# Optimization experiments

Measured on AMD Instinct MI355X. Metric: run time of the kernel, lower is better.

## Reference

```python
import jax, jax.numpy as jnp
import numpy as np

B, C, F = 8, 2048, 128


def setup_inputs() -> dict:
    key = jax.random.key(0)
    ks = jax.random.split(key, 13)
    features = jax.random.normal(ks[0], (B, C, F), dtype=jnp.float32)
    # sparse-ish boolean adjacency masks over operations
    pred_mask = jax.random.uniform(ks[1], (B, C, C)) < 0.05
    succ_mask = jax.random.uniform(ks[2], (B, C, C)) < 0.05
    same_type_mask = jax.random.uniform(ks[3], (B, C, C)) < 0.10

    def linear(k, fan_in, fan_out):
        kw, kb = jax.random.split(k)
        bound = 1.0 / np.sqrt(fan_in)
        W = jax.random.uniform(kw, (fan_in, fan_out), minval=-bound, maxval=bound, dtype=jnp.float32)
        b = jax.random.uniform(kb, (fan_out,), minval=-bound, maxval=bound, dtype=jnp.float32)
        return W, b

    W_enc, b_enc = linear(ks[4], F, 4 * F)
    W_space, b_space = linear(ks[5], 3 * F, F)
    W_same, b_same = linear(ks[6], 2 * F, F)
    W_mix, b_mix = linear(ks[7], 2 * F, F)
    return {
        "features": features,
        "pred_mask": pred_mask,
        "succ_mask": succ_mask,
        "same_type_mask": same_type_mask,
        "W_enc": W_enc, "b_enc": b_enc,
        "W_space": W_space, "b_space": b_space,
        "W_same": W_same, "b_same": b_same,
        "W_mix": W_mix, "b_mix": b_mix,
    }


def reference(features, pred_mask, succ_mask, same_type_mask,
              W_enc, b_enc, W_space, b_space, W_same, b_same, W_mix, b_mix):
    # encoder: [B,C,F] -> [B,C,4F], split into origin + 3 message features
    enc = features @ W_enc + b_enc
    origin, e_pred, e_succ, e_same = jnp.split(enc, 4, axis=-1)

    def masked_mean(mask, e):
        # original builds (B,C,C,F) broadcast product then sums over 'other';
        # mathematically this is mask @ e with a clamped-degree divisor.
        m = mask.astype(e.dtype)                         # [B,C,C]
        deg = jnp.maximum(m.sum(-1, keepdims=True), 1.0)  # [B,C,1]
        return jnp.einsum('bij,bjf->bif', m, e) / deg

    pred_f = masked_mean(pred_mask, e_pred)
    succ_f = masked_mean(succ_mask, e_succ)
    same_f = masked_mean(same_type_mask, e_same)

    space_mixed = jnp.concatenate([pred_f, origin, succ_f], axis=-1) @ W_space + b_space
    same_mixed = jnp.concatenate([origin, same_f], axis=-1) @ W_same + b_same
    return jnp.concatenate([space_mixed, same_mixed], axis=-1) @ W_mix + b_mix
```

## Files before the change

### kernel.cpp

```cpp
#include <hip/hip_runtime.h>
#include <stdint.h>

typedef unsigned int uint;
typedef unsigned short ushort;
typedef unsigned char uchar;
typedef __attribute__((ext_vector_type(8))) short bf16x8;
typedef __attribute__((ext_vector_type(4))) float f32x4;

__device__ __forceinline__ ushort f2bf(float f) {
  uint u = __builtin_bit_cast(uint, f);
  return (ushort)((u + 0x7FFFu + ((u >> 16) & 1u)) >> 16);
}

__device__ __forceinline__ bf16x8 cvt8(uint lo, uint hi, uint& cacc) {
  uint x0 = __builtin_amdgcn_perm(0u, lo, 0x04010400u);
  uint x1 = __builtin_amdgcn_perm(0u, lo, 0x04030402u);
  uint x2 = __builtin_amdgcn_perm(0u, hi, 0x04010400u);
  uint x3 = __builtin_amdgcn_perm(0u, hi, 0x04030402u);
  uint n0 = ((x0 + 0x00FF00FFu) >> 8) & 0x00010001u;
  uint n1 = ((x1 + 0x00FF00FFu) >> 8) & 0x00010001u;
  uint n2 = ((x2 + 0x00FF00FFu) >> 8) & 0x00010001u;
  uint n3 = ((x3 + 0x00FF00FFu) >> 8) & 0x00010001u;
  cacc += n0 + n1 + n2 + n3;
  uint4 o;
  o.x = n0 * 0x3F80u; o.y = n1 * 0x3F80u;
  o.z = n2 * 0x3F80u; o.w = n3 * 0x3F80u;
  return __builtin_bit_cast(bf16x8, o);
}

__device__ __forceinline__ bf16x8 cvt8w(uint4 a, uint4 b, uint& cnt) {
  bf16x8 r;
  r[0] = a.x ? (short)0x3F80 : (short)0; cnt += (a.x != 0u);
  r[1] = a.y ? (short)0x3F80 : (short)0; cnt += (a.y != 0u);
  r[2] = a.z ? (short)0x3F80 : (short)0; cnt += (a.z != 0u);
  r[3] = a.w ? (short)0x3F80 : (short)0; cnt += (a.w != 0u);
  r[4] = b.x ? (short)0x3F80 : (short)0; cnt += (b.x != 0u);
  r[5] = b.y ? (short)0x3F80 : (short)0; cnt += (b.y != 0u);
  r[6] = b.z ? (short)0x3F80 : (short)0; cnt += (b.z != 0u);
  r[7] = b.w ? (short)0x3F80 : (short)0; cnt += (b.w != 0u);
  return r;
}

__global__ __launch_bounds__(256) void k_detect(
    const uint4* __restrict__ m, int* __restrict__ esz_out) {
  __shared__ int s_ok;
  if (threadIdx.x == 0) s_ok = 1;
  __syncthreads();
  int ok = 1;
#pragma unroll
  for (int i = 0; i < 16; ++i) {
    uint4 v = m[i * 256 + threadIdx.x];
    if (!(v.x <= 1u || v.x == 0x3F800000u)) ok = 0;
    if (!(v.y <= 1u || v.y == 0x3F800000u)) ok = 0;
    if (!(v.z <= 1u || v.z == 0x3F800000u)) ok = 0;
    if (!(v.w <= 1u || v.w == 0x3F800000u)) ok = 0;
  }
  if (!ok) atomicAnd(&s_ok, 0);
  __syncthreads();
  if (threadIdx.x == 0) *esz_out = s_ok ? 4 : 1;
}

__global__ __launch_bounds__(256) void k_prep(
    const float4* __restrict__ fin, ushort* __restrict__ fout,
    const float* __restrict__ We, const float* __restrict__ Ws,
    const float* __restrict__ Wm, const float* __restrict__ Wx,
    ushort* __restrict__ Te, ushort* __restrict__ Ts,
    ushort* __restrict__ Tm, ushort* __restrict__ Tx) {
  const int tid = blockIdx.x * 256 + threadIdx.x;
  for (int i = tid; i < 524288; i += 180224) {
    float4 v = fin[i];
    ushort4 o;
    o.x = f2bf(v.x); o.y = f2bf(v.y); o.z = f2bf(v.z); o.w = f2bf(v.w);
    *(ushort4*)&fout[(size_t)i * 4] = o;
  }
  int i = tid;
  if (i < 65536) { int n = i >> 7, k = i & 127; Te[i] = f2bf(We[k * 512 + n]); return; }
  i -= 65536;
  if (i < 49152) { int n = i / 384, k = i - n * 384; Ts[i] = f2bf(Ws[k * 128 + n]); return; }
  i -= 49152;
  if (i < 32768) { int n = i >> 8, k = i & 255; Tm[i] = f2bf(Wm[k * 128 + n]); return; }
  i -= 32768;
  if (i < 32768) { int n = i >> 8, k = i & 255; Tx[i] = f2bf(Wx[k * 128 + n]); return; }
}

__global__ __launch_bounds__(256) void k_enc(
    const ushort* __restrict__ featbf, const ushort* __restrict__ WTe,
    const float* __restrict__ bias, ushort* __restrict__ origin,
    ushort* __restrict__ eT0, ushort* __restrict__ eT1, ushort* __restrict__ eT2) {
  const int t = threadIdx.x;
  const int gm0 = blockIdx.x * 64;
  const int y = blockIdx.y;
  const int lane = t & 63, wave = t >> 6;
  const int m0w = (wave >> 1) * 32, n0w = (wave & 1) * 64;
  const int quad = lane >> 4, lr = lane & 15;
  const ushort* a0p = featbf + (size_t)(gm0 + m0w + lr) * 128 + quad * 8;
  const ushort* a1p = a0p + 16 * 128;
  bf16x8 af0[4], af1[4];
#pragma unroll
  for (int kc = 0; kc < 4; ++kc) {
    af0[kc] = *(const bf16x8*)(a0p + kc * 32);
    af1[kc] = *(const bf16x8*)(a1p + kc * 32);
  }
  f32x4 acc[2][4] = {};
#pragma unroll
  for (int j = 0; j < 4; ++j) {
    const ushort* bp = WTe + (size_t)(y * 128 + n0w + j * 16 + lr) * 128 + quad * 8;
#pragma unroll
    for (int kc = 0; kc < 4; ++kc) {
      bf16x8 bv = *(const bf16x8*)(bp + kc * 32);
      acc[0][j] = __builtin_amdgcn_mfma_f32_16x16x32_bf16(af0[kc], bv, acc[0][j], 0, 0, 0);
      acc[1][j] = __builtin_amdgcn_mfma_f32_16x16x32_bf16(af1[kc], bv, acc[1][j], 0, 0, 0);
    }
  }
  if (y == 0) {
#pragma unroll
    for (int i = 0; i < 2; ++i)
#pragma unroll
      for (int j = 0; j < 4; ++j) {
        int n = n0w + j * 16 + lr;
        float bb = bias[n];
        int mb = gm0 + m0w + i * 16 + quad * 4;
#pragma unroll
        for (int r = 0; r < 4; ++r)
          origin[(size_t)(mb + r) * 128 + n] = f2bf(acc[i][j][r] + bb);
      }
  } else {
    ushort* eT = (y == 1) ? eT0 : (y == 2) ? eT1 : eT2;
#pragma unroll
    for (int i = 0; i < 2; ++i)
#pragma unroll
      for (int j = 0; j < 4; ++j) {
        int n = n0w + j * 16 + lr;
        float bb = bias[y * 128 + n];
        int mb = gm0 + m0w + i * 16 + quad * 4;
        ushort4 o;
        o.x = f2bf(acc[i][j][0] + bb);
        o.y = f2bf(acc[i][j][1] + bb);
        o.z = f2bf(acc[i][j][2] + bb);
        o.w = f2bf(acc[i][j][3] + bb);
        *(ushort4*)&eT[(size_t)n * 16384 + mb] = o;
      }
  }
}

__global__ __launch_bounds__(256, 3) void k_mm(
    const void* __restrict__ mp, const void* __restrict__ ms,
    const void* __restrict__ mt,
    const ushort* __restrict__ eT0, const ushort* __restrict__ eT1,
    const ushort* __restrict__ eT2,
    ushort* __restrict__ P, ushort* __restrict__ S, ushort* __restrict__ T,
    const int* __restrict__ esz_p) {
  __shared__ uint degs[64];
  const int t = threadIdx.x;
  const int mtile = blockIdx.x, b = blockIdx.y, mid = blockIdx.z;
  const void* mask = (mid == 0) ? mp : (mid == 1) ? ms : mt;
  const ushort* eT = (mid == 0) ? eT0 : (mid == 1) ? eT1 : eT2;
  ushort* outp = (mid == 0) ? P : (mid == 1) ? S : T;
  const int esz = *esz_p;
  const size_t rowbase = (size_t)b * 2048 + mtile * 64;
  const int lane = t & 63, wave = t >> 6;
  const int m0w = (wave >> 1) * 32, n0w = (wave & 1) * 64;
  const int quad = lane >> 4, lr = lane & 15;
  const int r0 = m0w + lr, r1 = m0w + 16 + lr;
  const ushort* bp0 = eT + (size_t)(n0w + lr) * 16384 + (size_t)b * 2048 + quad * 8;
  const ushort* bp1 = bp0 + 16 * 16384;
  const ushort* bp2 = bp0 + 32 * 16384;
  const ushort* bp3 = bp0 + 48 * 16384;
  f32x4 acc[2][4] = {};
  uint cacc0 = 0, cacc1 = 0;

  if (esz == 1) {
    const uchar* ma = (const uchar*)mask + (rowbase + r0) * 2048 + quad * 8;
    const uchar* mb = (const uchar*)mask + (rowbase + r1) * 2048 + quad * 8;
    uint2 ra0 = *(const uint2*)(ma);
    uint2 ra1 = *(const uint2*)(ma + 32);
    uint2 rb0 = *(const uint2*)(mb);
    uint2 rb1 = *(const uint2*)(mb + 32);
#pragma unroll 2
    for (int k0 = 0; k0 < 2048; k0 += 64) {
      uint2 na0 = {}, na1 = {}, nb0 = {}, nb1 = {};
      if (k0 + 64 < 2048) {
        na0 = *(const uint2*)(ma + k0 + 64);
        na1 = *(const uint2*)(ma + k0 + 96);
        nb0 = *(const uint2*)(mb + k0 + 64);
        nb1 = *(const uint2*)(mb + k0 + 96);
      }
#pragma unroll
      for (int kc = 0; kc < 2; ++kc) {
        bf16x8 bv0 = *(const bf16x8*)(bp0 + k0 + kc * 32);
        bf16x8 bv1 = *(const bf16x8*)(bp1 + k0 + kc * 32);
        bf16x8 bv2 = *(const bf16x8*)(bp2 + k0 + kc * 32);
        bf16x8 bv3 = *(const bf16x8*)(bp3 + k0 + kc * 32);
        uint2 wa = kc ? ra1 : ra0;
        uint2 wb = kc ? rb1 : rb0;
        bf16x8 a0 = cvt8(wa.x, wa.y, cacc0);
        bf16x8 a1 = cvt8(wb.x, wb.y, cacc1);
        acc[0][0] = __builtin_amdgcn_mfma_f32_16x16x32_bf16(a0, bv0, acc[0][0], 0, 0, 0);
        acc[1][0] = __builtin_amdgcn_mfma_f32_16x16x32_bf16(a1, bv0, acc[1][0], 0, 0, 0);
        acc[0][1] = __builtin_amdgcn_mfma_f32_16x16x32_bf16(a0, bv1, acc[0][1], 0, 0, 0);
        acc[1][1] = __builtin_amdgcn_mfma_f32_16x16x32_bf16(a1, bv1, acc[1][1], 0, 0, 0);
        acc[0][2] = __builtin_amdgcn_mfma_f32_16x16x32_bf16(a0, bv2, acc[0][2], 0, 0, 0);
        acc[1][2] = __builtin_amdgcn_mfma_f32_16x16x32_bf16(a1, bv2, acc[1][2], 0, 0, 0);
        acc[0][3] = __builtin_amdgcn_mfma_f32_16x16x32_bf16(a0, bv3, acc[0][3], 0, 0, 0);
        acc[1][3] = __builtin_amdgcn_mfma_f32_16x16x32_bf16(a1, bv3, acc[1][3], 0, 0, 0);
      }
      ra0 = na0; ra1 = na1; rb0 = nb0; rb1 = nb1;
    }
  } else {
    const uint* ma = (const uint*)mask + (rowbase + r0) * 2048 + quad * 8;
    const uint* mb = (const uint*)mask + (rowbase + r1) * 2048 + quad * 8;
    for (int k0 = 0; k0 < 2048; k0 += 64) {
#pragma unroll
      for (int kc = 0; kc < 2; ++kc) {
        uint4 wa0 = *(const uint4*)(ma + k0 + kc * 32);
        uint4 wa1 = *(const uint4*)(ma + k0 + kc * 32 + 4);
        uint4 wb0 = *(const uint4*)(mb + k0 + kc * 32);
        uint4 wb1 = *(const uint4*)(mb + k0 + kc * 32 + 4);
        bf16x8 bv0 = *(const bf16x8*)(bp0 + k0 + kc * 32);
        bf16x8 bv1 = *(const bf16x8*)(bp1 + k0 + kc * 32);
        bf16x8 bv2 = *(const bf16x8*)(bp2 + k0 + kc * 32);
        bf16x8 bv3 = *(const bf16x8*)(bp3 + k0 + kc * 32);
        bf16x8 a0 = cvt8w(wa0, wa1, cacc0);
        bf16x8 a1 = cvt8w(wb0, wb1, cacc1);
        acc[0][0] = __builtin_amdgcn_mfma_f32_16x16x32_bf16(a0, bv0, acc[0][0], 0, 0, 0);
        acc[1][0] = __builtin_amdgcn_mfma_f32_16x16x32_bf16(a1, bv0, acc[1][0], 0, 0, 0);
        acc[0][1] = __builtin_amdgcn_mfma_f32_16x16x32_bf16(a0, bv1, acc[0][1], 0, 0, 0);
        acc[1][1] = __builtin_amdgcn_mfma_f32_16x16x32_bf16(a1, bv1, acc[1][1], 0, 0, 0);
        acc[0][2] = __builtin_amdgcn_mfma_f32_16x16x32_bf16(a0, bv2, acc[0][2], 0, 0, 0);
        acc[1][2] = __builtin_amdgcn_mfma_f32_16x16x32_bf16(a1, bv2, acc[1][2], 0, 0, 0);
        acc[0][3] = __builtin_amdgcn_mfma_f32_16x16x32_bf16(a0, bv3, acc[0][3], 0, 0, 0);
        acc[1][3] = __builtin_amdgcn_mfma_f32_16x16x32_bf16(a1, bv3, acc[1][3], 0, 0, 0);
      }
    }
  }

  int c0, c1;
  if (esz == 1) {
    c0 = (int)((cacc0 & 0xFFFFu) + (cacc0 >> 16));
    c1 = (int)((cacc1 & 0xFFFFu) + (cacc1 >> 16));
  } else {
    c0 = (int)cacc0;
    c1 = (int)cacc1;
  }
  c0 += __shfl_xor(c0, 16); c0 += __shfl_xor(c0, 32);
  c1 += __shfl_xor(c1, 16); c1 += __shfl_xor(c1, 32);
  if ((wave & 1) == 0 && quad == 0) { degs[r0] = (uint)c0; degs[r1] = (uint)c1; }
  __syncthreads();

#pragma unroll
  for (int i = 0; i < 2; ++i)
#pragma unroll
    for (int r = 0; r < 4; ++r) {
      int ml = m0w + i * 16 + quad * 4 + r;
      uint d = degs[ml];
      float inv = 1.0f / (float)(d > 0u ? d : 1u);
#pragma unroll
      for (int j = 0; j < 4; ++j) {
        int n = n0w + j * 16 + lr;
        outp[(rowbase + ml) * 128 + n] = f2bf(acc[i][j][r] * inv);
      }
    }
}

__device__ __forceinline__ void gemm_body(
    const ushort* __restrict__ A0, const ushort* __restrict__ A1,
    const ushort* __restrict__ A2, const ushort* __restrict__ Bsrc,
    int bstride, int K, const float* __restrict__ bias,
    void* __restrict__ out, int out_f32, int gm0, int t) {
  const int lane = t & 63, wave = t >> 6;
  const int m0w = (wave >> 1) * 32, n0w = (wave & 1) * 64;
  const int quad = lane >> 4, lr = lane & 15;
  const ushort* bbase = Bsrc + (size_t)(n0w + lr) * bstride + quad * 8;
  f32x4 acc[2][4] = {};
  for (int k0 = 0; k0 < K; k0 += 64) {
    const int seg = k0 >> 7;
    const ushort* Ap = (seg == 0) ? A0 : (seg == 1) ? A1 : A2;
    const int ko = k0 & 127;
    const ushort* a0p = Ap + (size_t)(gm0 + m0w + lr) * 128 + ko + quad * 8;
    const ushort* a1p = a0p + 16 * 128;
#pragma unroll
    for (int kc = 0; kc < 2; ++kc) {
      bf16x8 av0 = *(const bf16x8*)(a0p + kc * 32);
      bf16x8 av1 = *(const bf16x8*)(a1p + kc * 32);
      bf16x8 b0 = *(const bf16x8*)(bbase + k0 + kc * 32);
      bf16x8 b1 = *(const bf16x8*)(bbase + (size_t)16 * bstride + k0 + kc * 32);
      bf16x8 b2 = *(const bf16x8*)(bbase + (size_t)32 * bstride + k0 + kc * 32);
      bf16x8 b3 = *(const bf16x8*)(bbase + (size_t)48 * bstride + k0 + kc * 32);
      acc[0][0] = __builtin_amdgcn_mfma_f32_16x16x32_bf16(av0, b0, acc[0][0], 0, 0, 0);
      acc[1][0] = __builtin_amdgcn_mfma_f32_16x16x32_bf16(av1, b0, acc[1][0], 0, 0, 0);
      acc[0][1] = __builtin_amdgcn_mfma_f32_16x16x32_bf16(av0, b1, acc[0][1], 0, 0, 0);
      acc[1][1] = __builtin_amdgcn_mfma_f32_16x16x32_bf16(av1, b1, acc[1][1], 0, 0, 0);
      acc[0][2] = __builtin_amdgcn_mfma_f32_16x16x32_bf16(av0, b2, acc[0][2], 0, 0, 0);
      acc[1][2] = __builtin_amdgcn_mfma_f32_16x16x32_bf16(av1, b2, acc[1][2], 0, 0, 0);
      acc[0][3] = __builtin_amdgcn_mfma_f32_16x16x32_bf16(av0, b3, acc[0][3], 0, 0, 0);
      acc[1][3] = __builtin_amdgcn_mfma_f32_16x16x32_bf16(av1, b3, acc[1][3], 0, 0, 0);
    }
  }
#pragma unroll
  for (int i = 0; i < 2; ++i)
#pragma unroll
    for (int j = 0; j < 4; ++j) {
      const int n = n0w + j * 16 + lr;
      const float bb = bias[n];
      const int mb = gm0 + m0w + i * 16 + quad * 4;
      if (out_f32) {
#pragma unroll
        for (int r = 0; r < 4; ++r)
          ((float*)out)[(size_t)(mb + r) * 128 + n] = acc[i][j][r] + bb;
      } else {
#pragma unroll
        for (int r = 0; r < 4; ++r)
          ((ushort*)out)[(size_t)(mb + r) * 128 + n] = f2bf(acc[i][j][r] + bb);
      }
    }
}

__global__ __launch_bounds__(256) void k_xy(
    const ushort* __restrict__ P, const ushort* __restrict__ origin,
    const ushort* __restrict__ S, const ushort* __restrict__ T,
    const ushort* __restrict__ WTs, const ushort* __restrict__ WTm,
    const float* __restrict__ bs, const float* __restrict__ bm,
    ushort* __restrict__ X, ushort* __restrict__ Y) {
  const int gm0 = blockIdx.x * 64;
  if (blockIdx.y == 0)
    gemm_body(P, origin, S, WTs, 384, 384, bs, X, 0, gm0, threadIdx.x);
  else
    gemm_body(origin, T, nullptr, WTm, 256, 256, bm, Y, 0, gm0, threadIdx.x);
}

__global__ __launch_bounds__(256) void k_mix(
    const ushort* __restrict__ X, const ushort* __restrict__ Y,
    const ushort* __restrict__ WTx, const float* __restrict__ bx,
    float* __restrict__ out) {
  gemm_body(X, Y, nullptr, WTx, 256, 256, bx, out, 1, blockIdx.x * 64, threadIdx.x);
}

extern "C" void kernel_launch(void* const* d_in, const int* in_sizes, int n_in,
                              void* d_out, int out_size, void* d_ws,
                              size_t ws_size, hipStream_t stream) {
  const float* features = (const float*)d_in[0];
  const void* pred = d_in[1];
  const void* succ = d_in[2];
  const void* same = d_in[3];
  const float* W_enc = (const float*)d_in[4];
  const float* b_enc = (const float*)d_in[5];
  const float* W_space = (const float*)d_in[6];
  const float* b_space = (const float*)d_in[7];
  const float* W_same = (const float*)d_in[8];
  const float* b_same = (const float*)d_in[9];
  const float* W_mix = (const float*)d_in[10];
  const float* b_mix = (const float*)d_in[11];

  const size_t M = 16384;
  ushort* w = (ushort*)d_ws;
  ushort* feat_bf = w;  w += M * 128;
  ushort* WT_enc = w;   w += 512 * 128;
  ushort* WT_space = w; w += 128 * 384;
  ushort* WT_same = w;  w += 128 * 256;
  ushort* WT_mix = w;   w += 128 * 256;
  ushort* origin = w;   w += M * 128;
  ushort* eT0 = w;      w += M * 128;
  ushort* eT1 = w;      w += M * 128;
  ushort* eT2 = w;      w += M * 128;
  ushort* P = w;        w += M * 128;
  ushort* S = w;        w += M * 128;
  ushort* T = w;        w += M * 128;
  ushort* X = w;        w += M * 128;
  ushort* Y = w;        w += M * 128;
  int* esz = (int*)w;

  k_detect<<<1, 256, 0, stream>>>((const uint4*)pred, esz);
  k_prep<<<704, 256, 0, stream>>>((const float4*)features, feat_bf,
                                  W_enc, W_space, W_same, W_mix,
                                  WT_enc, WT_space, WT_same, WT_mix);
  k_enc<<<dim3(256, 4), 256, 0, stream>>>(feat_bf, WT_enc, b_enc,
                                          origin, eT0, eT1, eT2);
  k_mm<<<dim3(32, 8, 3), 256, 0, stream>>>(pred, succ, same, eT0, eT1, eT2,
                                           P, S, T, esz);
  k_xy<<<dim3(256, 2), 256, 0, stream>>>(P, origin, S, T, WT_space, WT_same,
                                         b_space, b_same, X, Y);
  k_mix<<<256, 256, 0, stream>>>(X, Y, WT_mix, b_mix, (float*)d_out);
}
```

Before: 500.3 us.

## Stage mask and embedding tiles through LDS with double-buffered async loads

The byte-mask path of k_mm now copies the B (transposed embedding) and A (mask) tiles into swizzled, double-buffered LDS using global_load_lds, and overlaps these loads with MFMA compute behind explicit waitcnt and barriers. The grid is flattened and remapped so that blocks sharing a panel are scheduled together, which should help L2 reuse. k_enc also transposes its output through swizzled LDS so the eT writes to global memory are coalesced. The cost is extra LDS use (about 36KB per block in k_mm), which may reduce occupancy, plus more barriers per iteration.

```diff
diff --git a/kernel.cpp b/kernel.cpp
--- a/kernel.cpp
+++ b/kernel.cpp
@@ -87,6 +87,7 @@
     const ushort* __restrict__ featbf, const ushort* __restrict__ WTe,
     const float* __restrict__ bias, ushort* __restrict__ origin,
     ushort* __restrict__ eT0, ushort* __restrict__ eT1, ushort* __restrict__ eT2) {
+  __shared__ ushort tr[128 * 64];
   const int t = threadIdx.x;
   const int gm0 = blockIdx.x * 64;
   const int y = blockIdx.y;
@@ -132,14 +133,25 @@
       for (int j = 0; j < 4; ++j) {
         int n = n0w + j * 16 + lr;
         float bb = bias[y * 128 + n];
-        int mb = gm0 + m0w + i * 16 + quad * 4;
+        int m_lo = m0w + i * 16 + quad * 4;
+        int chunk = m_lo >> 3;
+        int byteo = n * 128 + ((chunk ^ (n & 7)) << 4) + (m_lo & 7) * 2;
         ushort4 o;
         o.x = f2bf(acc[i][j][0] + bb);
         o.y = f2bf(acc[i][j][1] + bb);
         o.z = f2bf(acc[i][j][2] + bb);
         o.w = f2bf(acc[i][j][3] + bb);
-        *(ushort4*)&eT[(size_t)n * 16384 + mb] = o;
+        *(ushort4*)((char*)tr + byteo) = o;
       }
+    __syncthreads();
+    const int n = t >> 1, half = t & 1;
+    ushort* gp = eT + (size_t)n * 16384 + gm0 + half * 32;
+#pragma unroll
+    for (int cc = 0; cc < 4; ++cc) {
+      int c = half * 4 + cc;
+      uint4 v = *(const uint4*)((char*)tr + n * 128 + ((c ^ (n & 7)) << 4));
+      *(uint4*)&gp[cc * 8] = v;
+    }
   }
 }
 
@@ -150,9 +162,15 @@
     const ushort* __restrict__ eT2,
     ushort* __restrict__ P, ushort* __restrict__ S, ushort* __restrict__ T,
     const int* __restrict__ esz_p) {
+  __shared__ ushort Bs[2][8192];
+  __shared__ uchar As1[2][4096];
   __shared__ uint degs[64];
   const int t = threadIdx.x;
-  const int mtile = blockIdx.x, b = blockIdx.y, mid = blockIdx.z;
+  const int g = blockIdx.x;
+  const int X = g & 7, seq = g >> 3;
+  const int pl = seq >> 5, mtile = seq & 31;
+  const int panel = pl * 8 + X;
+  const int b = panel / 3, mid = panel - b * 3;
   const void* mask = (mid == 0) ? mp : (mid == 1) ? ms : mt;
   const ushort* eT = (mid == 0) ? eT0 : (mid == 1) ? eT1 : eT2;
   ushort* outp = (mid == 0) ? P : (mid == 1) ? S : T;
@@ -162,51 +180,112 @@
   const int m0w = (wave >> 1) * 32, n0w = (wave & 1) * 64;
   const int quad = lane >> 4, lr = lane & 15;
   const int r0 = m0w + lr, r1 = m0w + 16 + lr;
-  const ushort* bp0 = eT + (size_t)(n0w + lr) * 16384 + (size_t)b * 2048 + quad * 8;
-  const ushort* bp1 = bp0 + 16 * 16384;
-  const ushort* bp2 = bp0 + 32 * 16384;
-  const ushort* bp3 = bp0 + 48 * 16384;
   f32x4 acc[2][4] = {};
   uint cacc0 = 0, cacc1 = 0;
 
   if (esz == 1) {
-    const uchar* ma = (const uchar*)mask + (rowbase + r0) * 2048 + quad * 8;
-    const uchar* mb = (const uchar*)mask + (rowbase + r1) * 2048 + quad * 8;
-    uint2 ra0 = *(const uint2*)(ma);
-    uint2 ra1 = *(const uint2*)(ma + 32);
-    uint2 rb0 = *(const uint2*)(mb);
-    uint2 rb1 = *(const uint2*)(mb + 32);
-#pragma unroll 2
-    for (int k0 = 0; k0 < 2048; k0 += 64) {
-      uint2 na0 = {}, na1 = {}, nb0 = {}, nb1 = {};
-      if (k0 + 64 < 2048) {
-        na0 = *(const uint2*)(ma + k0 + 64);
-        na1 = *(const uint2*)(ma + k0 + 96);
-        nb0 = *(const uint2*)(mb + k0 + 64);
-        nb1 = *(const uint2*)(mb + k0 + 96);
-      }
-#pragma unroll
-      for (int kc = 0; kc < 2; ++kc) {
-        bf16x8 bv0 = *(const bf16x8*)(bp0 + k0 + kc * 32);
-        bf16x8 bv1 = *(const bf16x8*)(bp1 + k0 + kc * 32);
-        bf16x8 bv2 = *(const bf16x8*)(bp2 + k0 + kc * 32);
-        bf16x8 bv3 = *(const bf16x8*)(bp3 + k0 + kc * 32);
-        uint2 wa = kc ? ra1 : ra0;
-        uint2 wb = kc ? rb1 : rb0;
-        bf16x8 a0 = cvt8(wa.x, wa.y, cacc0);
-        bf16x8 a1 = cvt8(wb.x, wb.y, cacc1);
-        acc[0][0] = __builtin_amdgcn_mfma_f32_16x16x32_bf16(a0, bv0, acc[0][0], 0, 0, 0);
-        acc[1][0] = __builtin_amdgcn_mfma_f32_16x16x32_bf16(a1, bv0, acc[1][0], 0, 0, 0);
-        acc[0][1] = __builtin_amdgcn_mfma_f32_16x16x32_bf16(a0, bv1, acc[0][1], 0, 0, 0);
-        acc[1][1] = __builtin_amdgcn_mfma_f32_16x16x32_bf16(a1, bv1, acc[1][1], 0, 0, 0);
-        acc[0][2] = __builtin_amdgcn_mfma_f32_16x16x32_bf16(a0, bv2, acc[0][2], 0, 0, 0);
-        acc[1][2] = __builtin_amdgcn_mfma_f32_16x16x32_bf16(a1, bv2, acc[1][2], 0, 0, 0);
-        acc[0][3] = __builtin_amdgcn_mfma_f32_16x16x32_bf16(a0, bv3, acc[0][3], 0, 0, 0);
-        acc[1][3] = __builtin_amdgcn_mfma_f32_16x16x32_bf16(a1, bv3, acc[1][3], 0, 0, 0);
-      }
-      ra0 = na0; ra1 = na1; rb0 = nb0; rb1 = nb1;
-    }
+    const int cB = (lane & 7) ^ (lane >> 3);
+    const ushort* gsrcB = eT + (size_t)(wave * 32 + (lane >> 3)) * 16384 +
+                          (size_t)b * 2048 + cB * 8;
+    const int srow = wave * 16 + (lane >> 2);
+    const int cA = ((lane & 3) ^ (srow & 3)) << 4;
+    const uchar* gsrcA = (const uchar*)mask + (rowbase + srow) * 2048 + cA;
+    char* ldsB = (char*)Bs;
+    char* ldsA = (char*)As1;
+
+#define STAGEALL(BUF, K0)                                                     \
+  {                                                                           \
+    _Pragma("unroll") for (int ii = 0; ii < 4; ++ii)                          \
+        __builtin_amdgcn_global_load_lds(                                     \
+            (const __attribute__((address_space(1))) uint*)(gsrcB +           \
+                (size_t)ii * 131072 + (K0)),                                  \
+            (__attribute__((address_space(3))) uint*)(ldsB + (BUF) * 16384 +  \
+                wave * 4096 + ii * 1024 + lane * 16),                         \
+            16, 0, 0);                                                        \
+    __builtin_amdgcn_global_load_lds(                                         \
+        (const __attribute__((address_space(1))) uint*)(gsrcA + (K0)),        \
+        (__attribute__((address_space(3))) uint*)(ldsA + (BUF) * 4096 +       \
+            wave * 1024 + lane * 16),                                         \
+        16, 0, 0);                                                            \
+  }
+
+    const int s0 = quad ^ (lr & 7);
+    const int rowb0 = (n0w + 0 * 16 + lr) * 128 + (s0 << 4);
+    const int rowb1 = (n0w + 1 * 16 + lr) * 128 + (s0 << 4);
+    const int rowb2 = (n0w + 2 * 16 + lr) * 128 + (s0 << 4);
+    const int rowb3 = (n0w + 3 * 16 + lr) * 128 + (s0 << 4);
+    const int aA0 = r0 * 64 + ((((quad >> 1) ^ (lr & 3))) << 4) + (quad & 1) * 8;
+    const int aB0 = aA0 + 16 * 64;
+
+#define COMPUTE(BUF)                                                          \
+  {                                                                           \
+    const char* bb = (const char*)Bs + (BUF) * 16384;                         \
+    const char* ab = (const char*)As1 + (BUF) * 4096;                         \
+    uint2 wa0 = *(const uint2*)(ab + aA0);                                    \
+    uint2 wa1 = *(const uint2*)(ab + (aA0 ^ 32));                             \
+    uint2 wb0 = *(const uint2*)(ab + aB0);                                    \
+    uint2 wb1 = *(const uint2*)(ab + (aB0 ^ 32));                             \
+    bf16x8 b00 = *(const bf16x8*)(bb + rowb0);                                \
+    bf16x8 b10 = *(const bf16x8*)(bb + rowb1);                                \
+    bf16x8 b20 = *(const bf16x8*)(bb + rowb2);                                \
+    bf16x8 b30 = *(const bf16x8*)(bb + rowb3);                                \
+    bf16x8 b01 = *(const bf16x8*)(bb + (rowb0 ^ 64));                         \
+    bf16x8 b11 = *(const bf16x8*)(bb + (rowb1 ^ 64));                         \
+    bf16x8 b21 = *(const bf16x8*)(bb + (rowb2 ^ 64));                         \
+    bf16x8 b31 = *(const bf16x8*)(bb + (rowb3 ^ 64));                         \
+    bf16x8 a0 = cvt8(wa0.x, wa0.y, cacc0);                                    \
+    bf16x8 a1 = cvt8(wb0.x, wb0.y, cacc1);                                    \
+    bf16x8 a0h = cvt8(wa1.x, wa1.y, cacc0);                                   \
+    bf16x8 a1h = cvt8(wb1.x, wb1.y, cacc1);                                   \
+    __builtin_amdgcn_s_setprio(1);                                            \
+    acc[0][0] = __builtin_amdgcn_mfma_f32_16x16x32_bf16(a0, b00, acc[0][0], 0, 0, 0); \
+    acc[1][0] = __builtin_amdgcn_mfma_f32_16x16x32_bf16(a1, b00, acc[1][0], 0, 0, 0); \
+    acc[0][1] = __builtin_amdgcn_mfma_f32_16x16x32_bf16(a0, b10, acc[0][1], 0, 0, 0); \
+    acc[1][1] = __builtin_amdgcn_mfma_f32_16x16x32_bf16(a1, b10, acc[1][1], 0, 0, 0); \
+    acc[0][2] = __builtin_amdgcn_mfma_f32_16x16x32_bf16(a0, b20, acc[0][2], 0, 0, 0); \
+    acc[1][2] = __builtin_amdgcn_mfma_f32_16x16x32_bf16(a1, b20, acc[1][2], 0, 0, 0); \
+    acc[0][3] = __builtin_amdgcn_mfma_f32_16x16x32_bf16(a0, b30, acc[0][3], 0, 0, 0); \
+    acc[1][3] = __builtin_amdgcn_mfma_f32_16x16x32_bf16(a1, b30, acc[1][3], 0, 0, 0); \
+    acc[0][0] = __builtin_amdgcn_mfma_f32_16x16x32_bf16(a0h, b01, acc[0][0], 0, 0, 0); \
+    acc[1][0] = __builtin_amdgcn_mfma_f32_16x16x32_bf16(a1h, b01, acc[1][0], 0, 0, 0); \
+    acc[0][1] = __builtin_amdgcn_mfma_f32_16x16x32_bf16(a0h, b11, acc[0][1], 0, 0, 0); \
+    acc[1][1] = __builtin_amdgcn_mfma_f32_16x16x32_bf16(a1h, b11, acc[1][1], 0, 0, 0); \
+    acc[0][2] = __builtin_amdgcn_mfma_f32_16x16x32_bf16(a0h, b21, acc[0][2], 0, 0, 0); \
+    acc[1][2] = __builtin_amdgcn_mfma_f32_16x16x32_bf16(a1h, b21, acc[1][2], 0, 0, 0); \
+    acc[0][3] = __builtin_amdgcn_mfma_f32_16x16x32_bf16(a0h, b31, acc[0][3], 0, 0, 0); \
+    acc[1][3] = __builtin_amdgcn_mfma_f32_16x16x32_bf16(a1h, b31, acc[1][3], 0, 0, 0); \
+    __builtin_amdgcn_s_setprio(0);                                            \
+  }
+
+#define KITER(BUF, VM)                                                        \
+  asm volatile("s_waitcnt vmcnt(" #VM ")" ::: "memory");                      \
+  __builtin_amdgcn_s_barrier();                                               \
+  __builtin_amdgcn_sched_barrier(0);                                          \
+  COMPUTE(BUF);                                                               \
+  asm volatile("" ::: "memory");                                              \
+  __builtin_amdgcn_s_barrier();
+
+    STAGEALL(0, 0)
+    STAGEALL(1, 64)
+    for (int k0 = 0; k0 < 1920; k0 += 128) {
+      KITER(0, 5)
+      STAGEALL(0, k0 + 128)
+      KITER(1, 5)
+      STAGEALL(1, k0 + 192)
+    }
+    KITER(0, 5)
+    asm volatile("s_waitcnt vmcnt(0)" ::: "memory");
+    __builtin_amdgcn_s_barrier();
+    __builtin_amdgcn_sched_barrier(0);
+    COMPUTE(1)
+#undef KITER
+#undef COMPUTE
+#undef STAGEALL
   } else {
+    const ushort* bp0 = eT + (size_t)(n0w + lr) * 16384 + (size_t)b * 2048 + quad * 8;
+    const ushort* bp1 = bp0 + 16 * 16384;
+    const ushort* bp2 = bp0 + 32 * 16384;
+    const ushort* bp3 = bp0 + 48 * 16384;
     const uint* ma = (const uint*)mask + (rowbase + r0) * 2048 + quad * 8;
     const uint* mb = (const uint*)mask + (rowbase + r1) * 2048 + quad * 8;
     for (int k0 = 0; k0 < 2048; k0 += 64) {
@@ -375,8 +454,8 @@
                                   WT_enc, WT_space, WT_same, WT_mix);
   k_enc<<<dim3(256, 4), 256, 0, stream>>>(feat_bf, WT_enc, b_enc,
                                           origin, eT0, eT1, eT2);
-  k_mm<<<dim3(32, 8, 3), 256, 0, stream>>>(pred, succ, same, eT0, eT1, eT2,
-                                           P, S, T, esz);
+  k_mm<<<768, 256, 0, stream>>>(pred, succ, same, eT0, eT1, eT2,
+                                P, S, T, esz);
   k_xy<<<dim3(256, 2), 256, 0, stream>>>(P, origin, S, T, WT_space, WT_same,
                                          b_space, b_same, X, Y);
   k_mix<<<256, 256, 0, stream>>>(X, Y, WT_mix, b_mix, (float*)d_out);
```

New measurement: 493.9 us. About the same (-1.3%).

## Split masked-mean GEMM into LDS-pipelined and register-pipelined kernels, stage encoder transpose

Applied to the files above, without the earlier changes.

The encoder now transposes its message outputs through a swizzled shared-memory tile, so each thread writes coalesced 16-byte chunks to the transposed eT buffers. The masked aggregation is split across two kernels, each handling half of the 24 batch-mask panels. The first uses global_load_lds into a triple-buffered, swizzled LDS pipeline with explicit waitcnt/barrier scheduling and raised MFMA priority. The second uses a double-buffered register prefetch of mask and embedding fragments. The aim is to hide global-load latency in the bandwidth-bound mask GEMM, at the cost of an extra kernel launch, two launches that run back to back rather than concurrently, and more LDS or register pressure.

```diff
diff --git a/kernel.cpp b/kernel.cpp
--- a/kernel.cpp
+++ b/kernel.cpp
@@ -87,6 +87,7 @@
     const ushort* __restrict__ featbf, const ushort* __restrict__ WTe,
     const float* __restrict__ bias, ushort* __restrict__ origin,
     ushort* __restrict__ eT0, ushort* __restrict__ eT1, ushort* __restrict__ eT2) {
+  __shared__ ushort tr[128 * 64];
   const int t = threadIdx.x;
   const int gm0 = blockIdx.x * 64;
   const int y = blockIdx.y;
@@ -132,18 +133,205 @@
       for (int j = 0; j < 4; ++j) {
         int n = n0w + j * 16 + lr;
         float bb = bias[y * 128 + n];
-        int mb = gm0 + m0w + i * 16 + quad * 4;
+        int m_lo = m0w + i * 16 + quad * 4;
+        int chunk = m_lo >> 3;
+        int byteo = n * 128 + ((chunk ^ (n & 7)) << 4) + (m_lo & 7) * 2;
         ushort4 o;
         o.x = f2bf(acc[i][j][0] + bb);
         o.y = f2bf(acc[i][j][1] + bb);
         o.z = f2bf(acc[i][j][2] + bb);
         o.w = f2bf(acc[i][j][3] + bb);
-        *(ushort4*)&eT[(size_t)n * 16384 + mb] = o;
+        *(ushort4*)((char*)tr + byteo) = o;
       }
-  }
-}
-
-__global__ __launch_bounds__(256, 3) void k_mm(
+    __syncthreads();
+    const int n = t >> 1, half = t & 1;
+    ushort* gp = eT + (size_t)n * 16384 + gm0 + half * 32;
+#pragma unroll
+    for (int cc = 0; cc < 4; ++cc) {
+      int c = half * 4 + cc;
+      uint4 v = *(const uint4*)((char*)tr + n * 128 + ((c ^ (n & 7)) << 4));
+      *(uint4*)&gp[cc * 8] = v;
+    }
+  }
+}
+
+__device__ __forceinline__ void mm_epilogue(
+    uint* degs, f32x4 acc[2][4], uint cacc0, uint cacc1, int esz,
+    int m0w, int n0w, int quad, int lr, int wave,
+    ushort* outp, size_t rowbase) {
+  const int r0 = m0w + lr, r1 = m0w + 16 + lr;
+  int c0, c1;
+  if (esz == 1) {
+    c0 = (int)((cacc0 & 0xFFFFu) + (cacc0 >> 16));
+    c1 = (int)((cacc1 & 0xFFFFu) + (cacc1 >> 16));
+  } else {
+    c0 = (int)cacc0;
+    c1 = (int)cacc1;
+  }
+  c0 += __shfl_xor(c0, 16); c0 += __shfl_xor(c0, 32);
+  c1 += __shfl_xor(c1, 16); c1 += __shfl_xor(c1, 32);
+  if ((wave & 1) == 0 && quad == 0) { degs[r0] = (uint)c0; degs[r1] = (uint)c1; }
+  __syncthreads();
+#pragma unroll
+  for (int i = 0; i < 2; ++i)
+#pragma unroll
+    for (int r = 0; r < 4; ++r) {
+      int ml = m0w + i * 16 + quad * 4 + r;
+      uint d = degs[ml];
+      float inv = 1.0f / (float)(d > 0u ? d : 1u);
+#pragma unroll
+      for (int j = 0; j < 4; ++j) {
+        int n = n0w + j * 16 + lr;
+        outp[(rowbase + ml) * 128 + n] = f2bf(acc[i][j][r] * inv);
+      }
+    }
+}
+
+__device__ __forceinline__ void mm_esz4(
+    const void* mask, const ushort* eT, size_t rowbase, int b,
+    int m0w, int n0w, int quad, int lr,
+    f32x4 acc[2][4], uint& cacc0, uint& cacc1) {
+  const int r0 = m0w + lr, r1 = m0w + 16 + lr;
+  const ushort* bp0 = eT + (size_t)(n0w + lr) * 16384 + (size_t)b * 2048 + quad * 8;
+  const ushort* bp1 = bp0 + 16 * 16384;
+  const ushort* bp2 = bp0 + 32 * 16384;
+  const ushort* bp3 = bp0 + 48 * 16384;
+  const uint* ma = (const uint*)mask + (rowbase + r0) * 2048 + quad * 8;
+  const uint* mb = (const uint*)mask + (rowbase + r1) * 2048 + quad * 8;
+  for (int k0 = 0; k0 < 2048; k0 += 64) {
+#pragma unroll
+    for (int kc = 0; kc < 2; ++kc) {
+      uint4 wa0 = *(const uint4*)(ma + k0 + kc * 32);
+      uint4 wa1 = *(const uint4*)(ma + k0 + kc * 32 + 4);
+      uint4 wb0 = *(const uint4*)(mb + k0 + kc * 32);
+      uint4 wb1 = *(const uint4*)(mb + k0 + kc * 32 + 4);
+      bf16x8 bv0 = *(const bf16x8*)(bp0 + k0 + kc * 32);
+      bf16x8 bv1 = *(const bf16x8*)(bp1 + k0 + kc * 32);
+      bf16x8 bv2 = *(const bf16x8*)(bp2 + k0 + kc * 32);
+      bf16x8 bv3 = *(const bf16x8*)(bp3 + k0 + kc * 32);
+      bf16x8 a0 = cvt8w(wa0, wa1, cacc0);
+      bf16x8 a1 = cvt8w(wb0, wb1, cacc1);
+      acc[0][0] = __builtin_amdgcn_mfma_f32_16x16x32_bf16(a0, bv0, acc[0][0], 0, 0, 0);
+      acc[1][0] = __builtin_amdgcn_mfma_f32_16x16x32_bf16(a1, bv0, acc[1][0], 0, 0, 0);
+      acc[0][1] = __builtin_amdgcn_mfma_f32_16x16x32_bf16(a0, bv1, acc[0][1], 0, 0, 0);
+      acc[1][1] = __builtin_amdgcn_mfma_f32_16x16x32_bf16(a1, bv1, acc[1][1], 0, 0, 0);
+      acc[0][2] = __builtin_amdgcn_mfma_f32_16x16x32_bf16(a0, bv2, acc[0][2], 0, 0, 0);
+      acc[1][2] = __builtin_amdgcn_mfma_f32_16x16x32_bf16(a1, bv2, acc[1][2], 0, 0, 0);
+      acc[0][3] = __builtin_amdgcn_mfma_f32_16x16x32_bf16(a0, bv3, acc[0][3], 0, 0, 0);
+      acc[1][3] = __builtin_amdgcn_mfma_f32_16x16x32_bf16(a1, bv3, acc[1][3], 0, 0, 0);
+    }
+  }
+}
+
+__global__ __launch_bounds__(256, 2) void k_mmA(
+    const void* __restrict__ mp, const void* __restrict__ ms,
+    const void* __restrict__ mt,
+    const ushort* __restrict__ eT0, const ushort* __restrict__ eT1,
+    const ushort* __restrict__ eT2,
+    ushort* __restrict__ P, ushort* __restrict__ S, ushort* __restrict__ T,
+    const int* __restrict__ esz_p) {
+  __shared__ __align__(16) char smem[61440];
+  const int t = threadIdx.x;
+  const int mtile = blockIdx.x;
+  const int panel = blockIdx.y;
+  const int b = panel / 3, mid = panel - b * 3;
+  const void* mask = (mid == 0) ? mp : (mid == 1) ? ms : mt;
+  const ushort* eT = (mid == 0) ? eT0 : (mid == 1) ? eT1 : eT2;
+  ushort* outp = (mid == 0) ? P : (mid == 1) ? S : T;
+  const int esz = *esz_p;
+  const size_t rowbase = (size_t)b * 2048 + mtile * 64;
+  const int lane = t & 63, wave = t >> 6;
+  const int m0w = (wave >> 1) * 32, n0w = (wave & 1) * 64;
+  const int quad = lane >> 4, lr = lane & 15;
+  f32x4 acc[2][4] = {};
+  uint cacc0 = 0, cacc1 = 0;
+
+  if (esz == 1) {
+    const int r0B = wave * 32 + (lane >> 3);
+    const ushort* gB = eT + (size_t)r0B * 16384 + (size_t)b * 2048 +
+                       ((lane & 7) ^ (r0B & 7)) * 8;
+    const int r0A = wave * 16 + (lane >> 2);
+    const uchar* gA = (const uchar*)mask + (size_t)(rowbase + r0A) * 2048 +
+                      (((lane & 3) ^ (r0A & 3)) << 4);
+
+#define STG(BUF, PH)                                                          \
+  {                                                                           \
+    _Pragma("unroll") for (int ii = 0; ii < 4; ++ii)                          \
+        __builtin_amdgcn_global_load_lds(                                     \
+            (const __attribute__((address_space(1))) uint*)(gB +              \
+                (size_t)ii * 8 * 16384 + (PH) * 64),                          \
+            (__attribute__((address_space(3))) uint*)(smem + (BUF) * 16384 +  \
+                wave * 4096 + ii * 1024 + lane * 16),                         \
+            16, 0, 0);                                                        \
+    __builtin_amdgcn_global_load_lds(                                         \
+        (const __attribute__((address_space(1))) uint*)(gA + (PH) * 64),      \
+        (__attribute__((address_space(3))) uint*)(smem + 49152 +              \
+            (BUF) * 4096 + wave * 1024 + lane * 16),                          \
+        16, 0, 0);                                                            \
+  }
+
+#define CPT(BUF)                                                              \
+  {                                                                           \
+    const char* Bb = smem + (BUF) * 16384;                                    \
+    const char* Ab = smem + 49152 + (BUF) * 4096;                             \
+    _Pragma("unroll") for (int kc = 0; kc < 2; ++kc) {                        \
+      const int ach = (((kc << 1) + (quad >> 1)) ^ (lr & 3)) << 4;            \
+      uint2 va0 = *(const uint2*)(Ab + (m0w + lr) * 64 + ach + (quad & 1) * 8); \
+      uint2 va1 = *(const uint2*)(Ab + (m0w + 16 + lr) * 64 + ach + (quad & 1) * 8); \
+      const int bch = (((kc << 2) + quad) ^ (lr & 7)) << 4;                   \
+      bf16x8 b0 = *(const bf16x8*)(Bb + (n0w + lr) * 128 + bch);              \
+      bf16x8 b1 = *(const bf16x8*)(Bb + (n0w + 16 + lr) * 128 + bch);         \
+      bf16x8 b2 = *(const bf16x8*)(Bb + (n0w + 32 + lr) * 128 + bch);         \
+      bf16x8 b3 = *(const bf16x8*)(Bb + (n0w + 48 + lr) * 128 + bch);         \
+      bf16x8 a0 = cvt8(va0.x, va0.y, cacc0);                                  \
+      bf16x8 a1 = cvt8(va1.x, va1.y, cacc1);                                  \
+      __builtin_amdgcn_s_setprio(1);                                          \
+      acc[0][0] = __builtin_amdgcn_mfma_f32_16x16x32_bf16(a0, b0, acc[0][0], 0, 0, 0); \
+      acc[1][0] = __builtin_amdgcn_mfma_f32_16x16x32_bf16(a1, b0, acc[1][0], 0, 0, 0); \
+      acc[0][1] = __builtin_amdgcn_mfma_f32_16x16x32_bf16(a0, b1, acc[0][1], 0, 0, 0); \
+      acc[1][1] = __builtin_amdgcn_mfma_f32_16x16x32_bf16(a1, b1, acc[1][1], 0, 0, 0); \
+      acc[0][2] = __builtin_amdgcn_mfma_f32_16x16x32_bf16(a0, b2, acc[0][2], 0, 0, 0); \
+      acc[1][2] = __builtin_amdgcn_mfma_f32_16x16x32_bf16(a1, b2, acc[1][2], 0, 0, 0); \
+      acc[0][3] = __builtin_amdgcn_mfma_f32_16x16x32_bf16(a0, b3, acc[0][3], 0, 0, 0); \
+      acc[1][3] = __builtin_amdgcn_mfma_f32_16x16x32_bf16(a1, b3, acc[1][3], 0, 0, 0); \
+      __builtin_amdgcn_s_setprio(0);                                          \
+    }                                                                         \
+  }
+
+#define ITER(BUF, VM)                                                         \
+  asm volatile("s_waitcnt vmcnt(" #VM ")" ::: "memory");                      \
+  __builtin_amdgcn_s_barrier();                                               \
+  __builtin_amdgcn_sched_barrier(0);                                          \
+  CPT(BUF);                                                                   \
+  asm volatile("" ::: "memory");                                              \
+  __builtin_amdgcn_s_barrier();                                               \
+  asm volatile("" ::: "memory");
+
+    STG(0, 0)
+    STG(1, 1)
+    STG(2, 2)
+    for (int ph = 0; ph < 27; ph += 3) {
+      ITER(0, 10) STG(0, ph + 3)
+      ITER(1, 10) STG(1, ph + 4)
+      ITER(2, 10) STG(2, ph + 5)
+    }
+    ITER(0, 10) STG(0, 30)
+    ITER(1, 10) STG(1, 31)
+    ITER(2, 10)
+    ITER(0, 5)
+    ITER(1, 0)
+#undef ITER
+#undef CPT
+#undef STG
+  } else {
+    mm_esz4(mask, eT, rowbase, b, m0w, n0w, quad, lr, acc, cacc0, cacc1);
+  }
+  __syncthreads();
+  mm_epilogue((uint*)smem, acc, cacc0, cacc1, esz, m0w, n0w, quad, lr, wave,
+              outp, rowbase);
+}
+
+__global__ __launch_bounds__(256, 3) void k_mmB(
     const void* __restrict__ mp, const void* __restrict__ ms,
     const void* __restrict__ mt,
     const ushort* __restrict__ eT0, const ushort* __restrict__ eT1,
@@ -152,7 +340,9 @@
     const int* __restrict__ esz_p) {
   __shared__ uint degs[64];
   const int t = threadIdx.x;
-  const int mtile = blockIdx.x, b = blockIdx.y, mid = blockIdx.z;
+  const int mtile = blockIdx.x;
+  const int panel = 12 + blockIdx.y;
+  const int b = panel / 3, mid = panel - b * 3;
   const void* mask = (mid == 0) ? mp : (mid == 1) ? ms : mt;
   const ushort* eT = (mid == 0) ? eT0 : (mid == 1) ? eT1 : eT2;
   ushort* outp = (mid == 0) ? P : (mid == 1) ? S : T;
@@ -161,105 +351,79 @@
   const int lane = t & 63, wave = t >> 6;
   const int m0w = (wave >> 1) * 32, n0w = (wave & 1) * 64;
   const int quad = lane >> 4, lr = lane & 15;
-  const int r0 = m0w + lr, r1 = m0w + 16 + lr;
-  const ushort* bp0 = eT + (size_t)(n0w + lr) * 16384 + (size_t)b * 2048 + quad * 8;
-  const ushort* bp1 = bp0 + 16 * 16384;
-  const ushort* bp2 = bp0 + 32 * 16384;
-  const ushort* bp3 = bp0 + 48 * 16384;
   f32x4 acc[2][4] = {};
   uint cacc0 = 0, cacc1 = 0;
 
   if (esz == 1) {
+    const int r0 = m0w + lr, r1 = m0w + 16 + lr;
     const uchar* ma = (const uchar*)mask + (rowbase + r0) * 2048 + quad * 8;
     const uchar* mb = (const uchar*)mask + (rowbase + r1) * 2048 + quad * 8;
-    uint2 ra0 = *(const uint2*)(ma);
-    uint2 ra1 = *(const uint2*)(ma + 32);
-    uint2 rb0 = *(const uint2*)(mb);
-    uint2 rb1 = *(const uint2*)(mb + 32);
-#pragma unroll 2
-    for (int k0 = 0; k0 < 2048; k0 += 64) {
-      uint2 na0 = {}, na1 = {}, nb0 = {}, nb1 = {};
-      if (k0 + 64 < 2048) {
-        na0 = *(const uint2*)(ma + k0 + 64);
-        na1 = *(const uint2*)(ma + k0 + 96);
-        nb0 = *(const uint2*)(mb + k0 + 64);
-        nb1 = *(const uint2*)(mb + k0 + 96);
-      }
-#pragma unroll
-      for (int kc = 0; kc < 2; ++kc) {
-        bf16x8 bv0 = *(const bf16x8*)(bp0 + k0 + kc * 32);
-        bf16x8 bv1 = *(const bf16x8*)(bp1 + k0 + kc * 32);
-        bf16x8 bv2 = *(const bf16x8*)(bp2 + k0 + kc * 32);
-        bf16x8 bv3 = *(const bf16x8*)(bp3 + k0 + kc * 32);
-        uint2 wa = kc ? ra1 : ra0;
-        uint2 wb = kc ? rb1 : rb0;
-        bf16x8 a0 = cvt8(wa.x, wa.y, cacc0);
-        bf16x8 a1 = cvt8(wb.x, wb.y, cacc1);
-        acc[0][0] = __builtin_amdgcn_mfma_f32_16x16x32_bf16(a0, bv0, acc[0][0], 0, 0, 0);
-        acc[1][0] = __builtin_amdgcn_mfma_f32_16x16x32_bf16(a1, bv0, acc[1][0], 0, 0, 0);
-        acc[0][1] = __builtin_amdgcn_mfma_f32_16x16x32_bf16(a0, bv1, acc[0][1], 0, 0, 0);
-        acc[1][1] = __builtin_amdgcn_mfma_f32_16x16x32_bf16(a1, bv1, acc[1][1], 0, 0, 0);
-        acc[0][2] = __builtin_amdgcn_mfma_f32_16x16x32_bf16(a0, bv2, acc[0][2], 0, 0, 0);
-        acc[1][2] = __builtin_amdgcn_mfma_f32_16x16x32_bf16(a1, bv2, acc[1][2], 0, 0, 0);
-        acc[0][3] = __builtin_amdgcn_mfma_f32_16x16x32_bf16(a0, bv3, acc[0][3], 0, 0, 0);
-        acc[1][3] = __builtin_amdgcn_mfma_f32_16x16x32_bf16(a1, bv3, acc[1][3], 0, 0, 0);
-      }
-      ra0 = na0; ra1 = na1; rb0 = nb0; rb1 = nb1;
-    }
+    const ushort* bp0 = eT + (size_t)(n0w + lr) * 16384 + (size_t)b * 2048 + quad * 8;
+    const ushort* bp1 = bp0 + 16 * 16384;
+    const ushort* bp2 = bp0 + 32 * 16384;
+    const ushort* bp3 = bp0 + 48 * 16384;
+    uint2 a00, a01, a10, a11;
+    uint2 c00, c01, c10, c11;
+    bf16x8 B0[8], B1[8];
+
+#define LDA0(K)                                                               \
+  { a00 = *(const uint2*)(ma + (K)); a01 = *(const uint2*)(ma + (K) + 32);    \
+    a10 = *(const uint2*)(mb + (K)); a11 = *(const uint2*)(mb + (K) + 32); }
+#define LDA1(K)                                                               \
+  { c00 = *(const uint2*)(ma + (K)); c01 = *(const uint2*)(ma + (K) + 32);    \
+    c10 = *(const uint2*)(mb + (K)); c11 = *(const uint2*)(mb + (K) + 32); }
+#define LDB(ARR, K)                                                           \
+  { ARR[0] = *(const bf16x8*)(bp0 + (K));      ARR[1] = *(const bf16x8*)(bp1 + (K)); \
+    ARR[2] = *(const bf16x8*)(bp2 + (K));      ARR[3] = *(const bf16x8*)(bp3 + (K)); \
+    ARR[4] = *(const bf16x8*)(bp0 + (K) + 32); ARR[5] = *(const bf16x8*)(bp1 + (K) + 32); \
+    ARR[6] = *(const bf16x8*)(bp2 + (K) + 32); ARR[7] = *(const bf16x8*)(bp3 + (K) + 32); }
+#define CPTR(A00, A01, A10, A11, BB)                                          \
+  {                                                                           \
+    bf16x8 a0 = cvt8((A00).x, (A00).y, cacc0);                                \
+    bf16x8 a1 = cvt8((A10).x, (A10).y, cacc1);                                \
+    acc[0][0] = __builtin_amdgcn_mfma_f32_16x16x32_bf16(a0, BB[0], acc[0][0], 0, 0, 0); \
+    acc[1][0] = __builtin_amdgcn_mfma_f32_16x16x32_bf16(a1, BB[0], acc[1][0], 0, 0, 0); \
+    acc[0][1] = __builtin_amdgcn_mfma_f32_16x16x32_bf16(a0, BB[1], acc[0][1], 0, 0, 0); \
+    acc[1][1] = __builtin_amdgcn_mfma_f32_16x16x32_bf16(a1, BB[1], acc[1][1], 0, 0, 0); \
+    acc[0][2] = __builtin_amdgcn_mfma_f32_16x16x32_bf16(a0, BB[2], acc[0][2], 0, 0, 0); \
+    acc[1][2] = __builtin_amdgcn_mfma_f32_16x16x32_bf16(a1, BB[2], acc[1][2], 0, 0, 0); \
+    acc[0][3] = __builtin_amdgcn_mfma_f32_16x16x32_bf16(a0, BB[3], acc[0][3], 0, 0, 0); \
+    acc[1][3] = __builtin_amdgcn_mfma_f32_16x16x32_bf16(a1, BB[3], acc[1][3], 0, 0, 0); \
+    bf16x8 a0h = cvt8((A01).x, (A01).y, cacc0);                               \
+    bf16x8 a1h = cvt8((A11).x, (A11).y, cacc1);                               \
+    acc[0][0] = __builtin_amdgcn_mfma_f32_16x16x32_bf16(a0h, BB[4], acc[0][0], 0, 0, 0); \
+    acc[1][0] = __builtin_amdgcn_mfma_f32_16x16x32_bf16(a1h, BB[4], acc[1][0], 0, 0, 0); \
+    acc[0][1] = __builtin_amdgcn_mfma_f32_16x16x32_bf16(a0h, BB[5], acc[0][1], 0, 0, 0); \
+    acc[1][1] = __builtin_amdgcn_mfma_f32_16x16x32_bf16(a1h, BB[5], acc[1][1], 0, 0, 0); \
+    acc[0][2] = __builtin_amdgcn_mfma_f32_16x16x32_bf16(a0h, BB[6], acc[0][2], 0, 0, 0); \
+    acc[1][2] = __builtin_amdgcn_mfma_f32_16x16x32_bf16(a1h, BB[6], acc[1][2], 0, 0, 0); \
+    acc[0][3] = __builtin_amdgcn_mfma_f32_16x16x32_bf16(a0h, BB[7], acc[0][3], 0, 0, 0); \
+    acc[1][3] = __builtin_amdgcn_mfma_f32_16x16x32_bf16(a1h, BB[7], acc[1][3], 0, 0, 0); \
+  }
+
+    LDA0(0)  LDB(B0, 0)
+    LDA1(64) LDB(B1, 64)
+    for (int k0 = 0; k0 < 1792; k0 += 128) {
+      CPTR(a00, a01, a10, a11, B0)
+      LDA0(k0 + 128) LDB(B0, k0 + 128)
+      CPTR(c00, c01, c10, c11, B1)
+      LDA1(k0 + 192) LDB(B1, k0 + 192)
+    }
+    CPTR(a00, a01, a10, a11, B0)
+    LDA0(1920) LDB(B0, 1920)
+    CPTR(c00, c01, c10, c11, B1)
+    LDA1(1984) LDB(B1, 1984)
+    CPTR(a00, a01, a10, a11, B0)
+    CPTR(c00, c01, c10, c11, B1)
+#undef CPTR
+#undef LDB
+#undef LDA1
+#undef LDA0
   } else {
-    const uint* ma = (const uint*)mask + (rowbase + r0) * 2048 + quad * 8;
-    const uint* mb = (const uint*)mask + (rowbase + r1) * 2048 + quad * 8;
-    for (int k0 = 0; k0 < 2048; k0 += 64) {
-#pragma unroll
-      for (int kc = 0; kc < 2; ++kc) {
-        uint4 wa0 = *(const uint4*)(ma + k0 + kc * 32);
-        uint4 wa1 = *(const uint4*)(ma + k0 + kc * 32 + 4);
-        uint4 wb0 = *(const uint4*)(mb + k0 + kc * 32);
-        uint4 wb1 = *(const uint4*)(mb + k0 + kc * 32 + 4);
-        bf16x8 bv0 = *(const bf16x8*)(bp0 + k0 + kc * 32);
-        bf16x8 bv1 = *(const bf16x8*)(bp1 + k0 + kc * 32);
-        bf16x8 bv2 = *(const bf16x8*)(bp2 + k0 + kc * 32);
-        bf16x8 bv3 = *(const bf16x8*)(bp3 + k0 + kc * 32);
-        bf16x8 a0 = cvt8w(wa0, wa1, cacc0);
-        bf16x8 a1 = cvt8w(wb0, wb1, cacc1);
-        acc[0][0] = __builtin_amdgcn_mfma_f32_16x16x32_bf16(a0, bv0, acc[0][0], 0, 0, 0);
-        acc[1][0] = __builtin_amdgcn_mfma_f32_16x16x32_bf16(a1, bv0, acc[1][0], 0, 0, 0);
-        acc[0][1] = __builtin_amdgcn_mfma_f32_16x16x32_bf16(a0, bv1, acc[0][1], 0, 0, 0);
-        acc[1][1] = __builtin_amdgcn_mfma_f32_16x16x32_bf16(a1, bv1, acc[1][1], 0, 0, 0);
-        acc[0][2] = __builtin_amdgcn_mfma_f32_16x16x32_bf16(a0, bv2, acc[0][2], 0, 0, 0);
-        acc[1][2] = __builtin_amdgcn_mfma_f32_16x16x32_bf16(a1, bv2, acc[1][2], 0, 0, 0);
-        acc[0][3] = __builtin_amdgcn_mfma_f32_16x16x32_bf16(a0, bv3, acc[0][3], 0, 0, 0);
-        acc[1][3] = __builtin_amdgcn_mfma_f32_16x16x32_bf16(a1, bv3, acc[1][3], 0, 0, 0);
-      }
-    }
-  }
-
-  int c0, c1;
-  if (esz == 1) {
-    c0 = (int)((cacc0 & 0xFFFFu) + (cacc0 >> 16));
-    c1 = (int)((cacc1 & 0xFFFFu) + (cacc1 >> 16));
-  } else {
-    c0 = (int)cacc0;
-    c1 = (int)cacc1;
-  }
-  c0 += __shfl_xor(c0, 16); c0 += __shfl_xor(c0, 32);
-  c1 += __shfl_xor(c1, 16); c1 += __shfl_xor(c1, 32);
-  if ((wave & 1) == 0 && quad == 0) { degs[r0] = (uint)c0; degs[r1] = (uint)c1; }
-  __syncthreads();
-
-#pragma unroll
-  for (int i = 0; i < 2; ++i)
-#pragma unroll
-    for (int r = 0; r < 4; ++r) {
-      int ml = m0w + i * 16 + quad * 4 + r;
-      uint d = degs[ml];
-      float inv = 1.0f / (float)(d > 0u ? d : 1u);
-#pragma unroll
-      for (int j = 0; j < 4; ++j) {
-        int n = n0w + j * 16 + lr;
-        outp[(rowbase + ml) * 128 + n] = f2bf(acc[i][j][r] * inv);
-      }
-    }
+    mm_esz4(mask, eT, rowbase, b, m0w, n0w, quad, lr, acc, cacc0, cacc1);
+  }
+  mm_epilogue(degs, acc, cacc0, cacc1, esz, m0w, n0w, quad, lr, wave,
+              outp, rowbase);
 }
 
 __device__ __forceinline__ void gemm_body(
@@ -375,8 +539,10 @@
                                   WT_enc, WT_space, WT_same, WT_mix);
   k_enc<<<dim3(256, 4), 256, 0, stream>>>(feat_bf, WT_enc, b_enc,
                                           origin, eT0, eT1, eT2);
-  k_mm<<<dim3(32, 8, 3), 256, 0, stream>>>(pred, succ, same, eT0, eT1, eT2,
-                                           P, S, T, esz);
+  k_mmA<<<dim3(32, 12), 256, 0, stream>>>(pred, succ, same, eT0, eT1, eT2,
+                                          P, S, T, esz);
+  k_mmB<<<dim3(32, 12), 256, 0, stream>>>(pred, succ, same, eT0, eT1, eT2,
+                                          P, S, T, esz);
   k_xy<<<dim3(256, 2), 256, 0, stream>>>(P, origin, S, T, WT_space, WT_same,
                                          b_space, b_same, X, Y);
   k_mix<<<256, 256, 0, stream>>>(X, Y, WT_mix, b_mix, (float*)d_out);
```

New measurement: 556.5 us. 11.2% more time.
